# Kernel optimization log

Hardware: AMD Instinct MI355X
Metric: run time of the kernel (lower is better)

Reference implementation:

```python
import jax, jax.numpy as jnp
import numpy as np

TAU = 0.05       # sinkhorn temperature (functools.partial in GCN_Net)
SK_ITERS = 20    # sinkhorn max_iter


def _mlp(x, w1, b1, w2, b2):
    # nn.Sequential(Linear, ReLU, Linear)
    return jnp.maximum(x @ w1 + b1, 0.0) @ w2 + b2


def _cosine(f1, f2, eps=1e-8):
    # torch CosineSimilarity over broadcast (E1,1,D) x (1,E2,D), computed as a GEMM
    n1 = jnp.maximum(jnp.linalg.norm(f1, axis=-1), eps)
    n2 = jnp.maximum(jnp.linalg.norm(f2, axis=-1), eps)
    return (f1 @ f2.T) / (n1[:, None] * n2[None, :])


def _sinkhorn(s):
    # log-domain sinkhorn, alternating row/col normalization (pygmtools-style)
    log_s = s / TAU
    for i in range(SK_ITERS):
        log_s = log_s - jax.nn.logsumexp(log_s, axis=(1 if i % 2 == 0 else 0), keepdims=True)
    return jnp.exp(log_s)


def _build_conn_edges(preds):
    # fully-connected off-diagonal graph; edge feats [dx, dy, dist, cls_src, cls_dst]
    n = preds.shape[0]
    pos = preds[:, 1:3]
    cls = preds[:, 6]
    idx = np.arange(n)
    r, c = np.meshgrid(idx, idx, indexing='ij')
    m = r != c
    conn = np.stack([r[m], c[m]], axis=1)  # (E,2), static under jit
    src, dst = conn[:, 0], conn[:, 1]
    d = pos[dst] - pos[src]                             # (E,2)
    dist = jnp.linalg.norm(d, axis=-1, keepdims=True)   # (E,1)
    edges = jnp.concatenate([d, dist, cls[src][:, None], cls[dst][:, None]], axis=-1)  # (E,5)
    return jnp.asarray(conn), edges


def _forward(ego_preds, cav_preds, node_w1, node_b1, node_w2, node_b2,
             edge_w1, edge_b1, edge_w2, edge_b2,
             l0_self_w, l0_self_b, l0_conv_w, l0_conv_b, l0_cls_w, l0_cls_b,
             l1_self_w, l1_self_b, l1_conv_w, l1_conv_b, l1_cls_w, l1_cls_b,
             fc_w, fc_b):
    ego = ego_preds[0]
    cav = cav_preds[0]
    n1, n2 = ego.shape[0], cav.shape[0]
    conn1, e1 = _build_conn_edges(ego)
    conn2, e2 = _build_conn_edges(cav)
    # --- NodeMLP affinity ---
    f1 = _mlp(ego[:, 1:6], node_w1, node_b1, node_w2, node_b2)
    f2 = _mlp(cav[:, 1:6], node_w1, node_b1, node_w2, node_b2)
    cls_eq = (ego[:, 6][:, None] == cav[:, 6][None, :]).astype(ego.dtype)
    conf = jnp.sum(jnp.sqrt(ego[:, 7:][:, None, :] * cav[:, 7:][None, :, :]), axis=-1)
    node_aff = cls_eq * conf * _cosine(f1, f2)                         # (n1,n2)
    # --- EdgeMLP affinity ---
    g1 = _mlp(e1[:, :3], edge_w1, edge_b1, edge_w2, edge_b2)
    g2 = _mlp(e2[:, :3], edge_w1, edge_b1, edge_w2, edge_b2)
    ecls = jnp.all(e1[:, 3:].astype(jnp.int32)[:, None, :] == e2[:, 3:].astype(jnp.int32)[None, :, :],
                   axis=-1).astype(ego.dtype)
    edge_aff = ecls * _cosine(g1, g2)                                  # (E1,E2)
    # --- Lawler affinity matrix K over association graph: node (i,a) -> i*n2+a ---
    N = n1 * n2
    rows = (conn1[:, 0][:, None] * n2 + conn2[:, 0][None, :]).ravel()
    cols = (conn1[:, 1][:, None] * n2 + conn2[:, 1][None, :]).ravel()
    K = jnp.zeros((N, N), ego.dtype).at[rows, cols].set(edge_aff.ravel())
    d_idx = jnp.arange(N)
    K = K.at[d_idx, d_idx].set(node_aff.ravel())
    # --- GCN adjacency = nonzero pattern of K, with added self-loops + sym norm ---
    A = (K != 0).astype(ego.dtype) + jnp.eye(N, dtype=ego.dtype)
    dinv = jax.lax.rsqrt(A.sum(axis=1))
    normA = dinv[:, None] * A * dinv[None, :]
    x = jnp.diag(K)[:, None]                                           # (N,1)
    # --- NGMConvLayers: self-loop Linear + GCNConv + sinkhorn channel ---
    for sw, sb, cw, cb, kw, kb in (
            (l0_self_w, l0_self_b, l0_conv_w, l0_conv_b, l0_cls_w, l0_cls_b),
            (l1_self_w, l1_self_b, l1_conv_w, l1_conv_b, l1_cls_w, l1_cls_b)):
        x = (x @ sw + sb) + (normA @ (x @ cw) + cb)
        sk = _sinkhorn((x @ kw + kb).reshape(n1, n2))
        x = x + sk.reshape(-1, 1)
    scores = x @ fc_w + fc_b                                           # (N,1)
    s = scores.reshape(n2, n1).T                                       # view(n2,-1).t()
    return _sinkhorn(s)


def setup_inputs() -> dict:
    key = jax.random.key(0)
    ks = jax.random.split(key, 16)

    def lin(k, fi, fo):
        kw, kb = jax.random.split(k)
        s = (2.0 / (fi + fo)) ** 0.5
        return (jax.random.normal(kw, (fi, fo), jnp.float32) * s,
                jax.random.normal(kb, (fo,), jnp.float32) * 0.01)

    def make_preds(k, n):
        k1, k2 = jax.random.split(k)
        p = jax.random.uniform(k1, (1, n, 8), jnp.float32)
        cls = jnp.floor(jax.random.uniform(k2, (1, n)) * 3.0)  # 3 discrete classes
        p = p.at[:, :, 6].set(cls)
        p = p.at[:, :, 7].set(0.1 + 0.9 * p[:, :, 7])          # positive confidences
        return p

    inp = {'ego_preds': make_preds(ks[0], 64), 'cav_preds': make_preds(ks[1], 64)}
    inp['node_w1'], inp['node_b1'] = lin(ks[2], 5, 64)
    inp['node_w2'], inp['node_b2'] = lin(ks[3], 64, 32)
    inp['edge_w1'], inp['edge_b1'] = lin(ks[4], 3, 64)
    inp['edge_w2'], inp['edge_b2'] = lin(ks[5], 64, 32)
    inp['l0_self_w'], inp['l0_self_b'] = lin(ks[6], 1, 16)
    inp['l0_conv_w'], inp['l0_conv_b'] = lin(ks[7], 1, 16)
    inp['l0_cls_w'], inp['l0_cls_b'] = lin(ks[8], 16, 1)
    inp['l1_self_w'], inp['l1_self_b'] = lin(ks[9], 16, 16)
    inp['l1_conv_w'], inp['l1_conv_b'] = lin(ks[10], 16, 16)
    inp['l1_cls_w'], inp['l1_cls_b'] = lin(ks[11], 16, 1)
    inp['fc_w'], inp['fc_b'] = lin(ks[12], 16, 1)
    return inp


def reference(ego_preds, cav_preds, node_w1, node_b1, node_w2, node_b2,
              edge_w1, edge_b1, edge_w2, edge_b2,
              l0_self_w, l0_self_b, l0_conv_w, l0_conv_b, l0_cls_w, l0_cls_b,
              l1_self_w, l1_self_b, l1_conv_w, l1_conv_b, l1_cls_w, l1_cls_b,
              fc_w, fc_b):
    return _forward(ego_preds, cav_preds, node_w1, node_b1, node_w2, node_b2,
                    edge_w1, edge_b1, edge_w2, edge_b2,
                    l0_self_w, l0_self_b, l0_conv_w, l0_conv_b, l0_cls_w, l0_cls_b,
                    l1_self_w, l1_self_b, l1_conv_w, l1_conv_b, l1_cls_w, l1_cls_b,
                    fc_w, fc_b)
```

## Files before the change

### kernel.cpp

```cpp
#include <hip/hip_runtime.h>
#include <math.h>


#define SK_SCALE 28.853900817779268f

template<int CTRL>
__device__ __forceinline__ float dppf(float x) {
    int xi = __float_as_int(x);
    int rr = __builtin_amdgcn_update_dpp(xi, xi, CTRL, 0xF, 0xF, false);
    return __int_as_float(rr);
}
__device__ __forceinline__ float quad_sum(float v) {
    v += dppf<0xB1>(v); v += dppf<0x4E>(v); return v;
}
__device__ __forceinline__ float quad_max(float v) {
    v = fmaxf(v, dppf<0xB1>(v)); v = fmaxf(v, dppf<0x4E>(v)); return v;
}
__device__ __forceinline__ float e2f(float x) { return __builtin_amdgcn_exp2f(x); }
__device__ __forceinline__ float rcpf(float x) { return __builtin_amdgcn_rcpf(x); }
__device__ __forceinline__ float dot4(const float4 a, const float4 b) {
    return a.x*b.x + a.y*b.y + a.z*b.z + a.w*b.w;
}
__device__ __forceinline__ void fma4(float4& a, float b, const float4 c) {
    a.x += b*c.x; a.y += b*c.y; a.z += b*c.z; a.w += b*c.w;
}
__device__ __forceinline__ void add4(float4& a, const float4 c) {
    a.x += c.x; a.y += c.y; a.z += c.z; a.w += c.w;
}
__device__ __forceinline__ void ld16(const float* p, float* o) {
    #pragma unroll
    for (int t = 0; t < 4; ++t) {
        float4 v = *(const float4*)(p + 4*t);
        o[4*t+0]=v.x; o[4*t+1]=v.y; o[4*t+2]=v.z; o[4*t+3]=v.w;
    }
}
__device__ __forceinline__ float dotsum16(const float* a, const float* b) {
    float s0=0,s1=0,s2=0,s3=0;
    #pragma unroll
    for (int t = 0; t < 4; ++t) {
        s0 += a[4*t+0]*b[4*t+0]; s1 += a[4*t+1]*b[4*t+1];
        s2 += a[4*t+2]*b[4*t+2]; s3 += a[4*t+3]*b[4*t+3];
    }
    return (s0+s1)+(s2+s3);
}
__device__ __forceinline__ float sum16(const float* a) {
    float s0=0,s1=0,s2=0,s3=0;
    #pragma unroll
    for (int t = 0; t < 4; ++t) {
        s0 += a[4*t+0]; s1 += a[4*t+1]; s2 += a[4*t+2]; s3 += a[4*t+3];
    }
    return (s0+s1)+(s2+s3);
}

__device__ __forceinline__ void sk_mult(const float* tq, const float* tt, int q, int r,
                                        float* up, float* vp, float* rmp,
                                        float* aq, float* att, float* u_out, float* v_out) {
    float rm = tq[0];
    #pragma unroll
    for (int m = 1; m < 16; ++m) rm = fmaxf(rm, tq[m]);
    rm = quad_max(rm);
    #pragma unroll
    for (int m = 0; m < 16; ++m) aq[m] = e2f(tq[m] - rm);
    float u = rcpf(quad_sum(sum16(aq)));
    if (q == 0) { rmp[r] = rm; up[r] = u; }
    __syncthreads();
    float rmq[16]; ld16(rmp + 16*q, rmq);
    #pragma unroll
    for (int m = 0; m < 16; ++m) att[m] = e2f(tt[m] - rmq[m]);
    float v;
    {
        float uq[16]; ld16(up + 16*q, uq);
        v = rcpf(quad_sum(dotsum16(att, uq)));
        if (q == 0) vp[r] = v;
        __syncthreads();
    }
    #pragma unroll 1
    for (int p = 0; p < 9; ++p) {
        float vq[16]; ld16(vp + 16*q, vq);
        u = rcpf(quad_sum(dotsum16(aq, vq)));
        if (q == 0) up[r] = u;
        __syncthreads();
        float uq[16]; ld16(up + 16*q, uq);
        v = rcpf(quad_sum(dotsum16(att, uq)));
        if (q == 0) vp[r] = v;
        __syncthreads();
    }
    *u_out = u; *v_out = v;
}

__device__ __forceinline__ void matvec_dual(const float* u1, const float* u1t,
                                            const float* u2, const float* u2t,
                                            const float* mmq, const float* dqv,
                                            const float* mmt, const float* dqt,
                                            float* o1, float* o1t, float* o2, float* o2t,
                                            int q, int r,
                                            float* WR1, float* WC1, float* WR2, float* WC2) {
    float rs1=0, rs2=0, cs1=0, cs2=0;
    #pragma unroll
    for (int m = 0; m < 16; ++m) {
        float md = mmq[m]*dqv[m], mdt = mmt[m]*dqt[m];
        rs1 += md * u1[m];               cs1 += mdt * u1t[m];
        rs2 += md * (u2 ? u2[m] : 1.0f); cs2 += mdt * (u2t ? u2t[m] : 1.0f);
    }
    rs1 = quad_sum(rs1); rs2 = quad_sum(rs2);
    cs1 = quad_sum(cs1); cs2 = quad_sum(cs2);
    if (q == 0) { WR1[r]=rs1; WR2[r]=rs2; WC1[r]=cs1; WC2[r]=cs2; }
    __syncthreads();
    float wr1[16], wc1[16], wr2[16], wc2[16];
    ld16(WR1 + 16*q, wr1); ld16(WC1 + 16*q, wc1);
    ld16(WR2 + 16*q, wr2); ld16(WC2 + 16*q, wc2);
    float W1 = quad_sum(sum16(wc1));
    float W2 = quad_sum(sum16(wc2));
    #pragma unroll
    for (int m = 0; m < 16; ++m) {
        float d = dqv[m], mm = mmq[m];
        float u1m = u1[m], u2m = u2 ? u2[m] : 1.0f;
        float z1 = mm*d*u1m, z2 = mm*d*u2m;
        o1[m] = d*((1.0f+mm)*d*u1m + mm*(W1 - rs1 - wc1[m] + z1));
        o2[m] = d*((1.0f+mm)*d*u2m + mm*(W2 - rs2 - wc2[m] + z2));
        float dt = dqt[m], mt = mmt[m];
        float u1tm = u1t[m], u2tm = u2t ? u2t[m] : 1.0f;
        float z1t = mt*dt*u1tm, z2t = mt*dt*u2tm;
        o1t[m] = dt*((1.0f+mt)*dt*u1tm + mt*(W1 - wr1[m] - cs1 + z1t));
        o2t[m] = dt*((1.0f+mt)*dt*u2tm + mt*(W2 - wr2[m] - cs2 + z2t));
    }
}

extern "C" __global__ __launch_bounds__(256, 1)
void gcn_match_kernel(const float* ego, const float* cav,
                      const float* nw1, const float* nb1, const float* nw2, const float* nb2,
                      const float* sw0, const float* sb0, const float* cw0, const float* cb0,
                      const float* kw0, const float* kb0,
                      const float* sw1, const float* sb1, const float* cw1, const float* cb1,
                      const float* kw1, const float* kb1,
                      const float* fcw, const float* fcb,
                      float* out) {
    __shared__ __align__(16) float sh_hT1[64 * 68];
    __shared__ __align__(16) float sh_hT2[64 * 68];
    __shared__ __align__(16) float sh_w2[2048];
    __shared__ __align__(16) float sh_f1[64 * 36];
    __shared__ __align__(16) float sh_f2[64 * 36];
    __shared__ __align__(16) float sh_nw1[320];
    __shared__ __align__(16) float sh_nb1[64], sh_nb2[32];
    __shared__ __align__(16) float sh_cls1[64], sh_cf1[64], sh_cls2[64], sh_cf2[64];
    __shared__ __align__(16) float sh_n1[64], sh_n2[64], sh_Dr[64], sh_Dc[64];
    __shared__ __align__(16) float sh_up[64], sh_vp[64], sh_rmp[64];
    __shared__ __align__(16) float sh_WR1[64], sh_WC1[64], sh_WR2[64], sh_WC2[64];
    __shared__ __align__(16) float sh_sw0[16], sh_sb0[16], sh_cw0[16], sh_cb0[16];
    __shared__ __align__(16) float sh_sb1[16], sh_cb1[16];
    __shared__ __align__(16) float sh_sw1[256], sh_cw1[256];
    __shared__ __align__(16) float sh_kw0[16], sh_kw1[16], sh_fcw[16];
    __shared__ float sh_kb[4];
    __shared__ float sh_avec[7 * 16];
    __shared__ float sh_coef[18];

    const int tid = threadIdx.x;
    const int wv = tid >> 6, lane = tid & 63;
    const int r = tid >> 2, q = tid & 3;

    ((float4*)sh_w2)[tid]       = ((const float4*)nw2)[tid];
    ((float4*)sh_w2)[tid + 256] = ((const float4*)nw2)[tid + 256];
    if (tid < 80)       ((float4*)sh_nw1)[tid]      = ((const float4*)nw1)[tid];
    else if (tid < 96)  ((float4*)sh_nb1)[tid-80]   = ((const float4*)nb1)[tid-80];
    else if (tid < 104) ((float4*)sh_nb2)[tid-96]   = ((const float4*)nb2)[tid-96];
    else if (tid < 108) ((float4*)sh_sw0)[tid-104]  = ((const float4*)sw0)[tid-104];
    else if (tid < 112) ((float4*)sh_sb0)[tid-108]  = ((const float4*)sb0)[tid-108];
    else if (tid < 116) ((float4*)sh_cw0)[tid-112]  = ((const float4*)cw0)[tid-112];
    else if (tid < 120) ((float4*)sh_cb0)[tid-116]  = ((const float4*)cb0)[tid-116];
    else if (tid < 124) ((float4*)sh_sb1)[tid-120]  = ((const float4*)sb1)[tid-120];
    else if (tid < 128) ((float4*)sh_cb1)[tid-124]  = ((const float4*)cb1)[tid-124];
    else if (tid < 192) ((float4*)sh_sw1)[tid-128]  = ((const float4*)sw1)[tid-128];
    else                ((float4*)sh_cw1)[tid-192]  = ((const float4*)cw1)[tid-192];
    if (tid < 4)        ((float4*)sh_kw0)[tid]      = ((const float4*)kw0)[tid];
    else if (tid < 8)   ((float4*)sh_kw1)[tid-4]    = ((const float4*)kw1)[tid-4];
    else if (tid < 12)  ((float4*)sh_fcw)[tid-8]    = ((const float4*)fcw)[tid-8];
    else if (tid == 12) sh_kb[0] = kb0[0];
    else if (tid == 13) sh_kb[1] = kb1[0];
    else if (tid == 14) sh_kb[2] = fcb[0];
    if (tid < 64) { sh_cls1[tid] = ego[tid*8+6]; sh_cf1[tid] = ego[tid*8+7]; }
    else if (tid < 128) { int j = tid-64; sh_cls2[j] = cav[j*8+6]; sh_cf2[j] = cav[j*8+7]; }
    __syncthreads();

    {
        float4 ea = ((const float4*)ego)[lane*2], eb = ((const float4*)ego)[lane*2+1];
        float4 ca = ((const float4*)cav)[lane*2], cb = ((const float4*)cav)[lane*2+1];
        #pragma unroll
        for (int kk = 0; kk < 16; ++kk) {
            int k = 16*wv + kk;
            float b1 = sh_nb1[k];
            float w0 = sh_nw1[k],       w1 = sh_nw1[64+k],  w2_ = sh_nw1[128+k];
            float w3 = sh_nw1[192+k],   w4 = sh_nw1[256+k];
            sh_hT1[k*68 + lane] = fmaxf(b1 + ea.y*w0 + ea.z*w1 + ea.w*w2_ + eb.x*w3 + eb.y*w4, 0.0f);
            sh_hT2[k*68 + lane] = fmaxf(b1 + ca.y*w0 + ca.z*w1 + ca.w*w2_ + cb.x*w3 + cb.y*w4, 0.0f);
        }
    }
    __syncthreads();

    if (wv < 2) {
        const float* HT = (wv == 0) ? sh_hT1 : sh_hT2;
        float* F  = (wv == 0) ? sh_f1 : sh_f2;
        float* NN = (wv == 0) ? sh_n1 : sh_n2;
        const int rr = lane >> 2, oq = lane & 3;
        float4 accA[4], accB[4];
        #pragma unroll
        for (int m = 0; m < 4; ++m) { accA[m] = make_float4(0,0,0,0); accB[m] = accA[m]; }
        #pragma unroll 4
        for (int k = 0; k < 64; ++k) {
            float4 hq = *(const float4*)(HT + k*68 + 4*rr);
            float4 wA = *(const float4*)(sh_w2 + k*32 + 4*oq);
            float4 wB = *(const float4*)(sh_w2 + k*32 + 16 + 4*oq);
            fma4(accA[0], hq.x, wA); fma4(accB[0], hq.x, wB);
            fma4(accA[1], hq.y, wA); fma4(accB[1], hq.y, wB);
            fma4(accA[2], hq.z, wA); fma4(accB[2], hq.z, wB);
            fma4(accA[3], hq.w, wA); fma4(accB[3], hq.w, wB);
        }
        float4 b2a = *(const float4*)(sh_nb2 + 4*oq);
        float4 b2b = *(const float4*)(sh_nb2 + 16 + 4*oq);
        float sq[4];
        #pragma unroll
        for (int m = 0; m < 4; ++m) {
            add4(accA[m], b2a); add4(accB[m], b2b);
            int row = 4*rr + m;
            *(float4*)(F + row*36 + 4*oq)      = accA[m];
            *(float4*)(F + row*36 + 16 + 4*oq) = accB[m];
            float q2 = dot4(accA[m], accA[m]) + dot4(accB[m], accB[m]);
            q2 += dppf<0xB1>(q2); q2 += dppf<0x4E>(q2);
            sq[m] = q2;
        }
        if (oq == 0) {
            #pragma unroll
            for (int m = 0; m < 4; ++m)
                NN[4*rr + m] = fmaxf(sqrtf(sq[m]), 1e-8f);
        }
    } else if (wv == 2) {
        if (lane < 16) {
            int o = lane;
            float ax=0, av=0, as_=0, aw=0, au=0, ae=0, a1=0;
            #pragma unroll
            for (int k = 0; k < 16; ++k) {
                float s0k = sh_sw0[k], c0k = sh_cw0[k], b0k = sh_sb0[k] + sh_cb0[k];
                float s1ko = sh_sw1[k*16+o], c1ko = sh_cw1[k*16+o];
                ax += s0k*s1ko;  av += c0k*s1ko + s0k*c1ko;  as_ += s1ko;
                aw += c0k*c1ko;  au += c1ko;  ae += b0k*c1ko;  a1 += b0k*s1ko;
            }
            a1 += sh_sb1[o] + sh_cb1[o];
            sh_avec[0*16+o]=ax; sh_avec[1*16+o]=av; sh_avec[2*16+o]=as_;
            sh_avec[3*16+o]=aw; sh_avec[4*16+o]=au; sh_avec[5*16+o]=ae;
            sh_avec[6*16+o]=a1;
        }
        if (lane < 18) {
            int t = lane; float c = 0.0f;
            if (t == 0)      { for (int k = 0; k < 16; ++k) c += sh_sw0[k]*sh_kw0[k]; }
            else if (t == 1) { for (int k = 0; k < 16; ++k) c += sh_cw0[k]*sh_kw0[k]; }
            else if (t == 2) { for (int k = 0; k < 16; ++k) c += (sh_sb0[k]+sh_cb0[k])*sh_kw0[k]; c += sh_kb[0]; }
            else if (t < 10) { int v = t-3;
                for (int o = 0; o < 16; ++o) c += sh_avec[v*16+o]*sh_kw1[o];
                if (v == 6) c += sh_kb[1];
            } else if (t < 17) { int v = t-10;
                for (int o = 0; o < 16; ++o) c += sh_avec[v*16+o]*sh_fcw[o];
                if (v == 6) c += sh_kb[2];
            } else { for (int o = 0; o < 16; ++o) c += sh_fcw[o]; }
            sh_coef[t] = c;
        }
    }
    __syncthreads();

    {
        const int sc = lane & 15, rc = lane >> 4;
        float dt[4][4];
        #pragma unroll
        for (int m = 0; m < 4; ++m)
            #pragma unroll
            for (int k = 0; k < 4; ++k) dt[m][k] = 0.0f;
        for (int kq = 0; kq < 8; ++kq) {
            float4 f2q[4];
            #pragma unroll
            for (int k = 0; k < 4; ++k)
                f2q[k] = *(const float4*)(sh_f2 + (sc + 16*k)*36 + 4*kq);
            #pragma unroll
            for (int m = 0; m < 4; ++m) {
                int rrow = 16*m + 4*wv + rc;
                float4 f1q = *(const float4*)(sh_f1 + rrow*36 + 4*kq);
                #pragma unroll
                for (int k = 0; k < 4; ++k) dt[m][k] += dot4(f1q, f2q[k]);
            }
        }
        #pragma unroll
        for (int m = 0; m < 4; ++m) {
            int rrow = 16*m + 4*wv + rc;
            #pragma unroll
            for (int k = 0; k < 4; ++k) {
                sh_hT1[rrow*68 + sc + 16*k] = dt[m][k];
                sh_hT2[(sc + 16*k)*68 + rrow] = dt[m][k];
            }
        }
    }
    float mmq[16], mmt[16], cfq[16], cft[16];
    float Drr, Dcr;
    {
        float c2q[16], c1q[16], f2v[16], f1v[16];
        ld16(sh_cls2 + 16*q, c2q); ld16(sh_cls1 + 16*q, c1q);
        ld16(sh_cf2 + 16*q, f2v);  ld16(sh_cf1 + 16*q, f1v);
        const float cls1r = sh_cls1[r], cls2r = sh_cls2[r];
        const float cf1r = sh_cf1[r],  cf2r  = sh_cf2[r];
        float dr = 0, dc = 0;
        #pragma unroll
        for (int m = 0; m < 16; ++m) {
            mmq[m] = (cls1r == c2q[m]) ? 1.0f : 0.0f;
            mmt[m] = (c1q[m] == cls2r) ? 1.0f : 0.0f;
            dr += mmq[m]; dc += mmt[m];
            cfq[m] = sqrtf(cf1r * f2v[m]);
            cft[m] = sqrtf(f1v[m] * cf2r);
        }
        Drr = quad_sum(dr);
        Dcr = quad_sum(dc);
        if (q == 0) { sh_Dr[r] = Drr; sh_Dc[r] = Dcr; }
    }
    __syncthreads();

    float dqv[16], dqt[16], x0[16], x0t[16];
    {
        float dcq[16], drq[16], n2q[16], n1q[16], dotq[16], dotTq[16];
        ld16(sh_Dc + 16*q, dcq); ld16(sh_Dr + 16*q, drq);
        ld16(sh_n2 + 16*q, n2q); ld16(sh_n1 + 16*q, n1q);
        ld16(sh_hT1 + r*68 + 16*q, dotq);
        ld16(sh_hT2 + r*68 + 16*q, dotTq);
        float Tdeg = quad_sum(sum16(dcq));
        const float n1r = sh_n1[r], n2r = sh_n2[r];
        #pragma unroll
        for (int m = 0; m < 16; ++m) {
            dqv[m] = (mmq[m] != 0.0f) ? (1.0f / sqrtf(Tdeg - Drr - dcq[m] + 3.0f)) : 1.0f;
            dqt[m] = (mmt[m] != 0.0f) ? (1.0f / sqrtf(Tdeg - drq[m] - Dcr + 3.0f)) : 1.0f;
            x0[m]  = mmq[m] * cfq[m] * (dotq[m]  / (n1r * n2q[m]));
            x0t[m] = mmt[m] * cft[m] * (dotTq[m] / (n1q[m] * n2r));
        }
    }

    float v0[16], v0t[16], oe[16], oet[16];
    matvec_dual(x0, x0t, nullptr, nullptr, mmq, dqv, mmt, dqt,
                v0, v0t, oe, oet, q, r, sh_WR1, sh_WC1, sh_WR2, sh_WC2);

    float t0q[16], t0t[16], t1b[16], t1bt[16], sbse[16], sbst[16];
    {
        float c0 = sh_coef[0], c1 = sh_coef[1], c2 = sh_coef[2];
        float ctx = sh_coef[3], ctv = sh_coef[4];
        float ce_ = sh_coef[8], ct1 = sh_coef[9];
        float csx = sh_coef[10], csv = sh_coef[11];
        float ce2 = sh_coef[15], cs1 = sh_coef[16];
        #pragma unroll
        for (int m = 0; m < 16; ++m) {
            t0q[m] = (c0*x0[m]  + c1*v0[m]  + c2) * SK_SCALE;
            t0t[m] = (c0*x0t[m] + c1*v0t[m] + c2) * SK_SCALE;
            t1b[m]  = ctx*x0[m]  + ctv*v0[m]  + ct1 + ce_*oe[m];
            t1bt[m] = ctx*x0t[m] + ctv*v0t[m] + ct1 + ce_*oet[m];
            sbse[m] = csx*x0[m]  + csv*v0[m]  + cs1 + ce2*oe[m];
            sbst[m] = csx*x0t[m] + csv*v0t[m] + cs1 + ce2*oet[m];
        }
    }

    float aq[16], att[16], u_, v_;
    sk_mult(t0q, t0t, q, r, sh_up, sh_vp, sh_rmp, aq, att, &u_, &v_);
    float s0v[16], s0t[16];
    {
        float vq[16], uq[16];
        ld16(sh_vp + 16*q, vq); ld16(sh_up + 16*q, uq);
        #pragma unroll
        for (int m = 0; m < 16; ++m) {
            s0v[m] = aq[m] * u_ * vq[m];
            s0t[m] = att[m] * uq[m] * v_;
        }
    }

    float ov[16], ovt[16], os[16], ost[16];
    matvec_dual(v0, v0t, s0v, s0t, mmq, dqv, mmt, dqt,
                ov, ovt, os, ost, q, r, sh_WR1, sh_WC1, sh_WR2, sh_WC2);
    float t1q[16], t1t[16], sacc[16], sacct[16];
    {
        float cts = sh_coef[5], cw_ = sh_coef[6], cu_ = sh_coef[7];
        float css = sh_coef[12], cw2 = sh_coef[13], cu2 = sh_coef[14];
        #pragma unroll
        for (int m = 0; m < 16; ++m) {
            t1q[m] = (t1b[m]  + cts*s0v[m] + cw_*ov[m]  + cu_*os[m])  * SK_SCALE;
            t1t[m] = (t1bt[m] + cts*s0t[m] + cw_*ovt[m] + cu_*ost[m]) * SK_SCALE;
            sacc[m]  = sbse[m] + css*s0v[m] + cw2*ov[m]  + cu2*os[m];
            sacct[m] = sbst[m] + css*s0t[m] + cw2*ovt[m] + cu2*ost[m];
        }
    }

    sk_mult(t1q, t1t, q, r, sh_up, sh_vp, sh_rmp, aq, att, &u_, &v_);
    {
        float c17 = sh_coef[17];
        float vq[16], uq[16];
        ld16(sh_vp + 16*q, vq); ld16(sh_up + 16*q, uq);
        #pragma unroll
        for (int m = 0; m < 16; ++m) {
            sacc[m]  += c17 * aq[m] * u_ * vq[m];
            sacct[m] += c17 * att[m] * uq[m] * v_;
        }
    }
    __syncthreads();

    {
        float t2q[16], t2t[16];
        #pragma unroll
        for (int m = 0; m < 16; ++m) {
            t2q[m] = sacct[m] * SK_SCALE;
            t2t[m] = sacc[m] * SK_SCALE;
        }
        sk_mult(t2q, t2t, q, r, sh_up, sh_vp, sh_rmp, aq, att, &u_, &v_);
        float vq[16]; ld16(sh_vp + 16*q, vq);
        #pragma unroll
        for (int t = 0; t < 4; ++t) {
            float4 o4;
            o4.x = aq[4*t+0] * u_ * vq[4*t+0];
            o4.y = aq[4*t+1] * u_ * vq[4*t+1];
            o4.z = aq[4*t+2] * u_ * vq[4*t+2];
            o4.w = aq[4*t+3] * u_ * vq[4*t+3];
            *(float4*)(out + r*64 + 16*q + 4*t) = o4;
        }
    }
}

extern "C" void kernel_launch(void* const* d_in, const int* in_sizes, int n_in,
                              void* d_out, int out_size, void* d_ws, size_t ws_size,
                              hipStream_t stream) {
    const float* ego = (const float*)d_in[0];
    const float* cav = (const float*)d_in[1];
    const float* nw1 = (const float*)d_in[2];
    const float* nb1 = (const float*)d_in[3];
    const float* nw2 = (const float*)d_in[4];
    const float* nb2 = (const float*)d_in[5];
    const float* sw0 = (const float*)d_in[10];
    const float* sb0 = (const float*)d_in[11];
    const float* cw0 = (const float*)d_in[12];
    const float* cb0 = (const float*)d_in[13];
    const float* kw0 = (const float*)d_in[14];
    const float* kb0 = (const float*)d_in[15];
    const float* sw1 = (const float*)d_in[16];
    const float* sb1 = (const float*)d_in[17];
    const float* cw1 = (const float*)d_in[18];
    const float* cb1 = (const float*)d_in[19];
    const float* kw1 = (const float*)d_in[20];
    const float* kb1 = (const float*)d_in[21];
    const float* fcw = (const float*)d_in[22];
    const float* fcb = (const float*)d_in[23];

    gcn_match_kernel<<<dim3(1), dim3(256), 0, stream>>>(
        ego, cav, nw1, nb1, nw2, nb2,
        sw0, sb0, cw0, cb0, kw0, kb0,
        sw1, sb1, cw1, cb1, kw1, kb1,
        fcw, fcb, (float*)d_out);
}
```

Before: 124.3 us.

## Run Sinkhorn iterations in a single wavefront to drop block-wide barriers

Each Sinkhorn solve now stages its 64x64 logits in shared memory, and one 64-lane wave does all the alternating row/column normalisations. Every lane holds a full row and a full column in registers, so the per-iteration __syncthreads across 256 threads goes away. The matvec is split into a single-vector version that is computed before the first Sinkhorn, and the mask/degree values are rebuilt afterwards to ease register pressure. The cost is that three waves sit idle during each Sinkhorn, each lane does 4x more serial arithmetic, and results are written back through shared memory.

```diff
diff --git a/kernel.cpp b/kernel.cpp
--- a/kernel.cpp
+++ b/kernel.cpp
@@ -13,9 +13,6 @@
 __device__ __forceinline__ float quad_sum(float v) {
     v += dppf<0xB1>(v); v += dppf<0x4E>(v); return v;
 }
-__device__ __forceinline__ float quad_max(float v) {
-    v = fmaxf(v, dppf<0xB1>(v)); v = fmaxf(v, dppf<0x4E>(v)); return v;
-}
 __device__ __forceinline__ float e2f(float x) { return __builtin_amdgcn_exp2f(x); }
 __device__ __forceinline__ float rcpf(float x) { return __builtin_amdgcn_rcpf(x); }
 __device__ __forceinline__ float dot4(const float4 a, const float4 b) {
@@ -34,15 +31,6 @@
         o[4*t+0]=v.x; o[4*t+1]=v.y; o[4*t+2]=v.z; o[4*t+3]=v.w;
     }
 }
-__device__ __forceinline__ float dotsum16(const float* a, const float* b) {
-    float s0=0,s1=0,s2=0,s3=0;
-    #pragma unroll
-    for (int t = 0; t < 4; ++t) {
-        s0 += a[4*t+0]*b[4*t+0]; s1 += a[4*t+1]*b[4*t+1];
-        s2 += a[4*t+2]*b[4*t+2]; s3 += a[4*t+3]*b[4*t+3];
-    }
-    return (s0+s1)+(s2+s3);
-}
 __device__ __forceinline__ float sum16(const float* a) {
     float s0=0,s1=0,s2=0,s3=0;
     #pragma unroll
@@ -52,55 +40,136 @@
     return (s0+s1)+(s2+s3);
 }
 
-__device__ __forceinline__ void sk_mult(const float* tq, const float* tt, int q, int r,
-                                        float* up, float* vp, float* rmp,
-                                        float* aq, float* att, float* u_out, float* v_out) {
-    float rm = tq[0];
-    #pragma unroll
-    for (int m = 1; m < 16; ++m) rm = fmaxf(rm, tq[m]);
-    rm = quad_max(rm);
-    #pragma unroll
-    for (int m = 0; m < 16; ++m) aq[m] = e2f(tq[m] - rm);
-    float u = rcpf(quad_sum(sum16(aq)));
-    if (q == 0) { rmp[r] = rm; up[r] = u; }
-    __syncthreads();
-    float rmq[16]; ld16(rmp + 16*q, rmq);
-    #pragma unroll
-    for (int m = 0; m < 16; ++m) att[m] = e2f(tt[m] - rmq[m]);
+__device__ void sk_wave(const float* An, const float* At, int lane,
+                        float* su, float* sv, float* srm) {
+    float a[64], b[64];
+    #pragma unroll
+    for (int t = 0; t < 16; ++t) {
+        float4 x = *(const float4*)(An + lane * 68 + 4 * t);
+        a[4*t+0]=x.x; a[4*t+1]=x.y; a[4*t+2]=x.z; a[4*t+3]=x.w;
+    }
+    #pragma unroll
+    for (int t = 0; t < 16; ++t) {
+        float4 y = *(const float4*)(At + lane * 68 + 4 * t);
+        b[4*t+0]=y.x; b[4*t+1]=y.y; b[4*t+2]=y.z; b[4*t+3]=y.w;
+    }
+    float m0 = fmaxf(a[0], a[1]), m1 = fmaxf(a[2], a[3]);
+    #pragma unroll
+    for (int j = 4; j < 64; j += 4) {
+        m0 = fmaxf(m0, fmaxf(a[j], a[j+1]));
+        m1 = fmaxf(m1, fmaxf(a[j+2], a[j+3]));
+    }
+    const float rm = fmaxf(m0, m1);
+    float s0=0, s1=0, s2=0, s3=0;
+    #pragma unroll
+    for (int j = 0; j < 64; j += 4) {
+        a[j]   = e2f(a[j]   - rm); s0 += a[j];
+        a[j+1] = e2f(a[j+1] - rm); s1 += a[j+1];
+        a[j+2] = e2f(a[j+2] - rm); s2 += a[j+2];
+        a[j+3] = e2f(a[j+3] - rm); s3 += a[j+3];
+    }
+    float u = rcpf((s0 + s1) + (s2 + s3));
+    srm[lane] = rm;
+    su[lane]  = u;
+    #pragma unroll
+    for (int t = 0; t < 16; ++t) {
+        float4 rv = *(const float4*)(srm + 4 * t);
+        b[4*t+0] = e2f(b[4*t+0] - rv.x);
+        b[4*t+1] = e2f(b[4*t+1] - rv.y);
+        b[4*t+2] = e2f(b[4*t+2] - rv.z);
+        b[4*t+3] = e2f(b[4*t+3] - rv.w);
+    }
     float v;
     {
-        float uq[16]; ld16(up + 16*q, uq);
-        v = rcpf(quad_sum(dotsum16(att, uq)));
-        if (q == 0) vp[r] = v;
-        __syncthreads();
+        float c0=0,c1=0,c2=0,c3=0;
+        #pragma unroll
+        for (int t = 0; t < 16; ++t) {
+            float4 uv = *(const float4*)(su + 4 * t);
+            c0 += b[4*t+0]*uv.x; c1 += b[4*t+1]*uv.y;
+            c2 += b[4*t+2]*uv.z; c3 += b[4*t+3]*uv.w;
+        }
+        v = rcpf((c0 + c1) + (c2 + c3));
+        sv[lane] = v;
     }
     #pragma unroll 1
     for (int p = 0; p < 9; ++p) {
-        float vq[16]; ld16(vp + 16*q, vq);
-        u = rcpf(quad_sum(dotsum16(aq, vq)));
-        if (q == 0) up[r] = u;
-        __syncthreads();
-        float uq[16]; ld16(up + 16*q, uq);
-        v = rcpf(quad_sum(dotsum16(att, uq)));
-        if (q == 0) vp[r] = v;
-        __syncthreads();
-    }
-    *u_out = u; *v_out = v;
+        {
+            float c0=0,c1=0,c2=0,c3=0;
+            #pragma unroll
+            for (int t = 0; t < 16; ++t) {
+                float4 vv = *(const float4*)(sv + 4 * t);
+                c0 += a[4*t+0]*vv.x; c1 += a[4*t+1]*vv.y;
+                c2 += a[4*t+2]*vv.z; c3 += a[4*t+3]*vv.w;
+            }
+            u = rcpf((c0 + c1) + (c2 + c3));
+            su[lane] = u;
+        }
+        {
+            float c0=0,c1=0,c2=0,c3=0;
+            #pragma unroll
+            for (int t = 0; t < 16; ++t) {
+                float4 uv = *(const float4*)(su + 4 * t);
+                c0 += b[4*t+0]*uv.x; c1 += b[4*t+1]*uv.y;
+                c2 += b[4*t+2]*uv.z; c3 += b[4*t+3]*uv.w;
+            }
+            v = rcpf((c0 + c1) + (c2 + c3));
+            sv[lane] = v;
+        }
+    }
+}
+
+__device__ __forceinline__ void recon_s(const float* A, const float* B,
+        const float* su, const float* sv, const float* srm,
+        int q, int r, float coef, float* sn, float* st) {
+    float tA[16], tB[16], uq[16], vq[16], rmq[16];
+    ld16(A + r*68 + 16*q, tA); ld16(B + r*68 + 16*q, tB);
+    ld16(su + 16*q, uq); ld16(sv + 16*q, vq); ld16(srm + 16*q, rmq);
+    const float cu = coef * su[r] * 1.0f;
+    const float cv = coef * sv[r];
+    const float rmr = srm[r];
+    #pragma unroll
+    for (int m = 0; m < 16; ++m) {
+        sn[m] = e2f(tA[m] - rmr) * cu * vq[m];
+        st[m] = e2f(tB[m] - rmq[m]) * uq[m] * cv;
+    }
+}
+
+__device__ __forceinline__ void matvec_one(const float* u1, const float* u1t,
+        const float* mmq, const float* dqv, const float* mmt, const float* dqt,
+        float* o1, float* o1t, int q, int r, float* WR, float* WC) {
+    float rs = 0, cs = 0;
+    #pragma unroll
+    for (int m = 0; m < 16; ++m) {
+        rs += mmq[m] * dqv[m] * u1[m];
+        cs += mmt[m] * dqt[m] * u1t[m];
+    }
+    rs = quad_sum(rs); cs = quad_sum(cs);
+    if (q == 0) { WR[r] = rs; WC[r] = cs; }
+    __syncthreads();
+    float wr[16], wc[16];
+    ld16(WR + 16*q, wr); ld16(WC + 16*q, wc);
+    float W = quad_sum(sum16(wc));
+    #pragma unroll
+    for (int m = 0; m < 16; ++m) {
+        float d = dqv[m], mm = mmq[m];
+        float z = mm * d * u1[m];
+        o1[m] = d * ((1.0f+mm)*d*u1[m] + mm*(W - rs - wc[m] + z));
+        float dt = dqt[m], mt = mmt[m];
+        float zt = mt * dt * u1t[m];
+        o1t[m] = dt * ((1.0f+mt)*dt*u1t[m] + mt*(W - wr[m] - cs + zt));
+    }
 }
 
 __device__ __forceinline__ void matvec_dual(const float* u1, const float* u1t,
-                                            const float* u2, const float* u2t,
-                                            const float* mmq, const float* dqv,
-                                            const float* mmt, const float* dqt,
-                                            float* o1, float* o1t, float* o2, float* o2t,
-                                            int q, int r,
-                                            float* WR1, float* WC1, float* WR2, float* WC2) {
+        const float* mmq, const float* dqv, const float* mmt, const float* dqt,
+        float* o1, float* o1t, float* o2, float* o2t, int q, int r,
+        float* WR1, float* WC1, float* WR2, float* WC2) {
     float rs1=0, rs2=0, cs1=0, cs2=0;
     #pragma unroll
     for (int m = 0; m < 16; ++m) {
         float md = mmq[m]*dqv[m], mdt = mmt[m]*dqt[m];
-        rs1 += md * u1[m];               cs1 += mdt * u1t[m];
-        rs2 += md * (u2 ? u2[m] : 1.0f); cs2 += mdt * (u2t ? u2t[m] : 1.0f);
+        rs1 += md * u1[m];  cs1 += mdt * u1t[m];
+        rs2 += md;          cs2 += mdt;
     }
     rs1 = quad_sum(rs1); rs2 = quad_sum(rs2);
     cs1 = quad_sum(cs1); cs2 = quad_sum(cs2);
@@ -114,15 +183,31 @@
     #pragma unroll
     for (int m = 0; m < 16; ++m) {
         float d = dqv[m], mm = mmq[m];
-        float u1m = u1[m], u2m = u2 ? u2[m] : 1.0f;
-        float z1 = mm*d*u1m, z2 = mm*d*u2m;
-        o1[m] = d*((1.0f+mm)*d*u1m + mm*(W1 - rs1 - wc1[m] + z1));
-        o2[m] = d*((1.0f+mm)*d*u2m + mm*(W2 - rs2 - wc2[m] + z2));
+        float z1 = mm*d*u1[m], z2 = mm*d;
+        o1[m] = d*((1.0f+mm)*d*u1[m] + mm*(W1 - rs1 - wc1[m] + z1));
+        o2[m] = d*((1.0f+mm)*d       + mm*(W2 - rs2 - wc2[m] + z2));
         float dt = dqt[m], mt = mmt[m];
-        float u1tm = u1t[m], u2tm = u2t ? u2t[m] : 1.0f;
-        float z1t = mt*dt*u1tm, z2t = mt*dt*u2tm;
-        o1t[m] = dt*((1.0f+mt)*dt*u1tm + mt*(W1 - wr1[m] - cs1 + z1t));
-        o2t[m] = dt*((1.0f+mt)*dt*u2tm + mt*(W2 - wr2[m] - cs2 + z2t));
+        float z1t = mt*dt*u1t[m], z2t = mt*dt;
+        o1t[m] = dt*((1.0f+mt)*dt*u1t[m] + mt*(W1 - wr1[m] - cs1 + z1t));
+        o2t[m] = dt*((1.0f+mt)*dt       + mt*(W2 - wr2[m] - cs2 + z2t));
+    }
+}
+
+__device__ __forceinline__ void build_mmdq(const float* cls1, const float* cls2,
+        const float* Dr, const float* Dc, int q, int r,
+        float* mmq, float* mmt, float* dqv, float* dqt) {
+    float c2q[16], c1q[16], dcq[16], drq[16];
+    ld16(cls2 + 16*q, c2q); ld16(cls1 + 16*q, c1q);
+    ld16(Dc + 16*q, dcq);   ld16(Dr + 16*q, drq);
+    const float cls1r = cls1[r], cls2r = cls2[r];
+    const float Drr = Dr[r], Dcr = Dc[r];
+    float Tdeg = quad_sum(sum16(dcq));
+    #pragma unroll
+    for (int m = 0; m < 16; ++m) {
+        mmq[m] = (cls1r == c2q[m]) ? 1.0f : 0.0f;
+        mmt[m] = (c1q[m] == cls2r) ? 1.0f : 0.0f;
+        dqv[m] = (mmq[m] != 0.0f) ? (1.0f / sqrtf(Tdeg - Drr - dcq[m] + 3.0f)) : 1.0f;
+        dqt[m] = (mmt[m] != 0.0f) ? (1.0f / sqrtf(Tdeg - drq[m] - Dcr + 3.0f)) : 1.0f;
     }
 }
 
@@ -144,8 +229,9 @@
     __shared__ __align__(16) float sh_nb1[64], sh_nb2[32];
     __shared__ __align__(16) float sh_cls1[64], sh_cf1[64], sh_cls2[64], sh_cf2[64];
     __shared__ __align__(16) float sh_n1[64], sh_n2[64], sh_Dr[64], sh_Dc[64];
-    __shared__ __align__(16) float sh_up[64], sh_vp[64], sh_rmp[64];
+    __shared__ __align__(16) float sh_u[64], sh_v[64], sh_rm[64];
     __shared__ __align__(16) float sh_WR1[64], sh_WC1[64], sh_WR2[64], sh_WC2[64];
+    __shared__ __align__(16) float sh_WR3[64], sh_WC3[64];
     __shared__ __align__(16) float sh_sw0[16], sh_sb0[16], sh_cw0[16], sh_cb0[16];
     __shared__ __align__(16) float sh_sb1[16], sh_cb1[16];
     __shared__ __align__(16) float sh_sw1[256], sh_cw1[256];
@@ -157,6 +243,8 @@
     const int tid = threadIdx.x;
     const int wv = tid >> 6, lane = tid & 63;
     const int r = tid >> 2, q = tid & 3;
+    float* sh_A = sh_hT1;
+    float* sh_B = sh_hT2;
 
     ((float4*)sh_w2)[tid]       = ((const float4*)nw2)[tid];
     ((float4*)sh_w2)[tid + 256] = ((const float4*)nw2)[tid + 256];
@@ -188,8 +276,8 @@
         for (int kk = 0; kk < 16; ++kk) {
             int k = 16*wv + kk;
             float b1 = sh_nb1[k];
-            float w0 = sh_nw1[k],       w1 = sh_nw1[64+k],  w2_ = sh_nw1[128+k];
-            float w3 = sh_nw1[192+k],   w4 = sh_nw1[256+k];
+            float w0 = sh_nw1[k],     w1 = sh_nw1[64+k], w2_ = sh_nw1[128+k];
+            float w3 = sh_nw1[192+k], w4 = sh_nw1[256+k];
             sh_hT1[k*68 + lane] = fmaxf(b1 + ea.y*w0 + ea.z*w1 + ea.w*w2_ + eb.x*w3 + eb.y*w4, 0.0f);
             sh_hT2[k*68 + lane] = fmaxf(b1 + ca.y*w0 + ca.z*w1 + ca.w*w2_ + cb.x*w3 + cb.y*w4, 0.0f);
         }
@@ -295,127 +383,143 @@
             }
         }
     }
-    float mmq[16], mmt[16], cfq[16], cft[16];
-    float Drr, Dcr;
-    {
-        float c2q[16], c1q[16], f2v[16], f1v[16];
+    {
+        float c2q[16], c1q[16];
         ld16(sh_cls2 + 16*q, c2q); ld16(sh_cls1 + 16*q, c1q);
-        ld16(sh_cf2 + 16*q, f2v);  ld16(sh_cf1 + 16*q, f1v);
         const float cls1r = sh_cls1[r], cls2r = sh_cls2[r];
-        const float cf1r = sh_cf1[r],  cf2r  = sh_cf2[r];
         float dr = 0, dc = 0;
         #pragma unroll
         for (int m = 0; m < 16; ++m) {
-            mmq[m] = (cls1r == c2q[m]) ? 1.0f : 0.0f;
-            mmt[m] = (c1q[m] == cls2r) ? 1.0f : 0.0f;
-            dr += mmq[m]; dc += mmt[m];
-            cfq[m] = sqrtf(cf1r * f2v[m]);
-            cft[m] = sqrtf(f1v[m] * cf2r);
-        }
-        Drr = quad_sum(dr);
-        Dcr = quad_sum(dc);
-        if (q == 0) { sh_Dr[r] = Drr; sh_Dc[r] = Dcr; }
-    }
-    __syncthreads();
-
-    float dqv[16], dqt[16], x0[16], x0t[16];
-    {
-        float dcq[16], drq[16], n2q[16], n1q[16], dotq[16], dotTq[16];
-        ld16(sh_Dc + 16*q, dcq); ld16(sh_Dr + 16*q, drq);
-        ld16(sh_n2 + 16*q, n2q); ld16(sh_n1 + 16*q, n1q);
+            dr += (cls1r == c2q[m]) ? 1.0f : 0.0f;
+            dc += (c1q[m] == cls2r) ? 1.0f : 0.0f;
+        }
+        dr = quad_sum(dr); dc = quad_sum(dc);
+        if (q == 0) { sh_Dr[r] = dr; sh_Dc[r] = dc; }
+    }
+    __syncthreads();
+
+    float mmq[16], mmt[16], dqv[16], dqt[16];
+    build_mmdq(sh_cls1, sh_cls2, sh_Dr, sh_Dc, q, r, mmq, mmt, dqv, dqt);
+    float x0[16], x0t[16];
+    {
+        float f2v[16], f1v[16], n2q[16], n1q[16], dotq[16], dotTq[16];
+        ld16(sh_cf2 + 16*q, f2v); ld16(sh_cf1 + 16*q, f1v);
+        ld16(sh_n2 + 16*q, n2q);  ld16(sh_n1 + 16*q, n1q);
         ld16(sh_hT1 + r*68 + 16*q, dotq);
         ld16(sh_hT2 + r*68 + 16*q, dotTq);
-        float Tdeg = quad_sum(sum16(dcq));
         const float n1r = sh_n1[r], n2r = sh_n2[r];
+        const float cf1r = sh_cf1[r], cf2r = sh_cf2[r];
         #pragma unroll
         for (int m = 0; m < 16; ++m) {
-            dqv[m] = (mmq[m] != 0.0f) ? (1.0f / sqrtf(Tdeg - Drr - dcq[m] + 3.0f)) : 1.0f;
-            dqt[m] = (mmt[m] != 0.0f) ? (1.0f / sqrtf(Tdeg - drq[m] - Dcr + 3.0f)) : 1.0f;
-            x0[m]  = mmq[m] * cfq[m] * (dotq[m]  / (n1r * n2q[m]));
-            x0t[m] = mmt[m] * cft[m] * (dotTq[m] / (n1q[m] * n2r));
+            x0[m]  = mmq[m] * sqrtf(cf1r * f2v[m]) * (dotq[m]  / (n1r * n2q[m]));
+            x0t[m] = mmt[m] * sqrtf(f1v[m] * cf2r) * (dotTq[m] / (n1q[m] * n2r));
         }
     }
 
     float v0[16], v0t[16], oe[16], oet[16];
-    matvec_dual(x0, x0t, nullptr, nullptr, mmq, dqv, mmt, dqt,
+    matvec_dual(x0, x0t, mmq, dqv, mmt, dqt,
                 v0, v0t, oe, oet, q, r, sh_WR1, sh_WC1, sh_WR2, sh_WC2);
-
-    float t0q[16], t0t[16], t1b[16], t1bt[16], sbse[16], sbst[16];
+    float ov[16], ovt[16];
+    matvec_one(v0, v0t, mmq, dqv, mmt, dqt, ov, ovt, q, r, sh_WR3, sh_WC3);
+
+    float t1b[16], t1bt[16], sbq[16], sbt[16];
     {
         float c0 = sh_coef[0], c1 = sh_coef[1], c2 = sh_coef[2];
         float ctx = sh_coef[3], ctv = sh_coef[4];
-        float ce_ = sh_coef[8], ct1 = sh_coef[9];
+        float cw_ = sh_coef[6], ce_ = sh_coef[8], ct1 = sh_coef[9];
         float csx = sh_coef[10], csv = sh_coef[11];
-        float ce2 = sh_coef[15], cs1 = sh_coef[16];
+        float cw2 = sh_coef[13], ce2 = sh_coef[15], cs1 = sh_coef[16];
+        #pragma unroll
+        for (int t = 0; t < 4; ++t) {
+            float4 a4, b4;
+            a4.x = (c0*x0[4*t+0] + c1*v0[4*t+0] + c2) * SK_SCALE;
+            a4.y = (c0*x0[4*t+1] + c1*v0[4*t+1] + c2) * SK_SCALE;
+            a4.z = (c0*x0[4*t+2] + c1*v0[4*t+2] + c2) * SK_SCALE;
+            a4.w = (c0*x0[4*t+3] + c1*v0[4*t+3] + c2) * SK_SCALE;
+            b4.x = (c0*x0t[4*t+0] + c1*v0t[4*t+0] + c2) * SK_SCALE;
+            b4.y = (c0*x0t[4*t+1] + c1*v0t[4*t+1] + c2) * SK_SCALE;
+            b4.z = (c0*x0t[4*t+2] + c1*v0t[4*t+2] + c2) * SK_SCALE;
+            b4.w = (c0*x0t[4*t+3] + c1*v0t[4*t+3] + c2) * SK_SCALE;
+            *(float4*)(sh_A + r*68 + 16*q + 4*t) = a4;
+            *(float4*)(sh_B + r*68 + 16*q + 4*t) = b4;
+        }
         #pragma unroll
         for (int m = 0; m < 16; ++m) {
-            t0q[m] = (c0*x0[m]  + c1*v0[m]  + c2) * SK_SCALE;
-            t0t[m] = (c0*x0t[m] + c1*v0t[m] + c2) * SK_SCALE;
-            t1b[m]  = ctx*x0[m]  + ctv*v0[m]  + ct1 + ce_*oe[m];
-            t1bt[m] = ctx*x0t[m] + ctv*v0t[m] + ct1 + ce_*oet[m];
-            sbse[m] = csx*x0[m]  + csv*v0[m]  + cs1 + ce2*oe[m];
-            sbst[m] = csx*x0t[m] + csv*v0t[m] + cs1 + ce2*oet[m];
-        }
-    }
-
-    float aq[16], att[16], u_, v_;
-    sk_mult(t0q, t0t, q, r, sh_up, sh_vp, sh_rmp, aq, att, &u_, &v_);
+            t1b[m]  = ctx*x0[m]  + ctv*v0[m]  + ct1 + ce_*oe[m]  + cw_*ov[m];
+            t1bt[m] = ctx*x0t[m] + ctv*v0t[m] + ct1 + ce_*oet[m] + cw_*ovt[m];
+            sbq[m]  = csx*x0[m]  + csv*v0[m]  + cs1 + ce2*oe[m]  + cw2*ov[m];
+            sbt[m]  = csx*x0t[m] + csv*v0t[m] + cs1 + ce2*oet[m] + cw2*ovt[m];
+        }
+    }
+    __syncthreads();
+
+    if (wv == 0) sk_wave(sh_A, sh_B, lane, sh_u, sh_v, sh_rm);
+    __syncthreads();
+
     float s0v[16], s0t[16];
-    {
-        float vq[16], uq[16];
-        ld16(sh_vp + 16*q, vq); ld16(sh_up + 16*q, uq);
-        #pragma unroll
-        for (int m = 0; m < 16; ++m) {
-            s0v[m] = aq[m] * u_ * vq[m];
-            s0t[m] = att[m] * uq[m] * v_;
-        }
-    }
-
-    float ov[16], ovt[16], os[16], ost[16];
-    matvec_dual(v0, v0t, s0v, s0t, mmq, dqv, mmt, dqt,
-                ov, ovt, os, ost, q, r, sh_WR1, sh_WC1, sh_WR2, sh_WC2);
-    float t1q[16], t1t[16], sacc[16], sacct[16];
-    {
-        float cts = sh_coef[5], cw_ = sh_coef[6], cu_ = sh_coef[7];
-        float css = sh_coef[12], cw2 = sh_coef[13], cu2 = sh_coef[14];
-        #pragma unroll
-        for (int m = 0; m < 16; ++m) {
-            t1q[m] = (t1b[m]  + cts*s0v[m] + cw_*ov[m]  + cu_*os[m])  * SK_SCALE;
-            t1t[m] = (t1bt[m] + cts*s0t[m] + cw_*ovt[m] + cu_*ost[m]) * SK_SCALE;
-            sacc[m]  = sbse[m] + css*s0v[m] + cw2*ov[m]  + cu2*os[m];
-            sacct[m] = sbst[m] + css*s0t[m] + cw2*ovt[m] + cu2*ost[m];
-        }
-    }
-
-    sk_mult(t1q, t1t, q, r, sh_up, sh_vp, sh_rmp, aq, att, &u_, &v_);
-    {
-        float c17 = sh_coef[17];
-        float vq[16], uq[16];
-        ld16(sh_vp + 16*q, vq); ld16(sh_up + 16*q, uq);
-        #pragma unroll
-        for (int m = 0; m < 16; ++m) {
-            sacc[m]  += c17 * aq[m] * u_ * vq[m];
-            sacct[m] += c17 * att[m] * uq[m] * v_;
-        }
-    }
-    __syncthreads();
-
-    {
-        float t2q[16], t2t[16];
-        #pragma unroll
-        for (int m = 0; m < 16; ++m) {
-            t2q[m] = sacct[m] * SK_SCALE;
-            t2t[m] = sacc[m] * SK_SCALE;
-        }
-        sk_mult(t2q, t2t, q, r, sh_up, sh_vp, sh_rmp, aq, att, &u_, &v_);
-        float vq[16]; ld16(sh_vp + 16*q, vq);
+    recon_s(sh_A, sh_B, sh_u, sh_v, sh_rm, q, r, 1.0f, s0v, s0t);
+    build_mmdq(sh_cls1, sh_cls2, sh_Dr, sh_Dc, q, r, mmq, mmt, dqv, dqt);
+    float os[16], ost[16];
+    matvec_one(s0v, s0t, mmq, dqv, mmt, dqt, os, ost, q, r, sh_WR1, sh_WC1);
+    float sacc[16], sacct[16];
+    {
+        float cts = sh_coef[5], cu_ = sh_coef[7];
+        float css = sh_coef[12], cu2 = sh_coef[14];
+        #pragma unroll
+        for (int t = 0; t < 4; ++t) {
+            float4 a4, b4;
+            #pragma unroll
+            for (int e = 0; e < 4; ++e) {
+                int m = 4*t + e;
+                float tn = (t1b[m]  + cts*s0v[m] + cu_*os[m])  * SK_SCALE;
+                float tt = (t1bt[m] + cts*s0t[m] + cu_*ost[m]) * SK_SCALE;
+                (&a4.x)[e] = tn; (&b4.x)[e] = tt;
+                sacc[m]  = sbq[m] + css*s0v[m] + cu2*os[m];
+                sacct[m] = sbt[m] + css*s0t[m] + cu2*ost[m];
+            }
+            *(float4*)(sh_A + r*68 + 16*q + 4*t) = a4;
+            *(float4*)(sh_B + r*68 + 16*q + 4*t) = b4;
+        }
+    }
+    __syncthreads();
+
+    if (wv == 0) sk_wave(sh_A, sh_B, lane, sh_u, sh_v, sh_rm);
+    __syncthreads();
+
+    {
+        float s1v[16], s1t[16];
+        recon_s(sh_A, sh_B, sh_u, sh_v, sh_rm, q, r, sh_coef[17], s1v, s1t);
+        #pragma unroll
+        for (int t = 0; t < 4; ++t) {
+            float4 a4, b4;
+            #pragma unroll
+            for (int e = 0; e < 4; ++e) {
+                int m = 4*t + e;
+                sacc[m]  += s1v[m];
+                sacct[m] += s1t[m];
+                (&a4.x)[e] = sacct[m] * SK_SCALE;
+                (&b4.x)[e] = sacc[m] * SK_SCALE;
+            }
+            *(float4*)(sh_A + r*68 + 16*q + 4*t) = a4;
+            *(float4*)(sh_B + r*68 + 16*q + 4*t) = b4;
+        }
+    }
+    __syncthreads();
+
+    if (wv == 0) sk_wave(sh_A, sh_B, lane, sh_u, sh_v, sh_rm);
+    __syncthreads();
+    {
+        float tA[16], vq[16];
+        ld16(sh_A + r*68 + 16*q, tA);
+        ld16(sh_v + 16*q, vq);
+        const float rmr = sh_rm[r], ur = sh_u[r];
         #pragma unroll
         for (int t = 0; t < 4; ++t) {
             float4 o4;
-            o4.x = aq[4*t+0] * u_ * vq[4*t+0];
-            o4.y = aq[4*t+1] * u_ * vq[4*t+1];
-            o4.z = aq[4*t+2] * u_ * vq[4*t+2];
-            o4.w = aq[4*t+3] * u_ * vq[4*t+3];
+            o4.x = e2f(tA[4*t+0] - rmr) * ur * vq[4*t+0];
+            o4.y = e2f(tA[4*t+1] - rmr) * ur * vq[4*t+1];
+            o4.z = e2f(tA[4*t+2] - rmr) * ur * vq[4*t+2];
+            o4.w = e2f(tA[4*t+3] - rmr) * ur * vq[4*t+3];
             *(float4*)(out + r*64 + 16*q + 4*t) = o4;
         }
     }
```

Result: slower. 146.1 us (+17.5%).
